# Performance work log

Hardware: AMD Instinct MI355X
Metric: run time of the kernel (lower is better)

Reference implementation:

```python
import jax, jax.numpy as jnp
import numpy as np

N_NODES = 50000
N_EDGES = 800000
IN_FEATS = 128
N_HEADS = 4
OUT_FEATS = 32
NEG_SLOPE = 0.01  # F.leaky_relu default


def setup_inputs() -> dict:
    key = jax.random.key(0)
    k1, k2, k3, k4, k5, k6 = jax.random.split(key, 6)
    feat = jax.random.normal(k1, (N_NODES, IN_FEATS), dtype=jnp.float32)
    src = jax.random.randint(k2, (N_EDGES,), 0, N_NODES, dtype=jnp.int64)
    dst = jax.random.randint(k3, (N_EDGES,), 0, N_NODES, dtype=jnp.int64)
    # xavier-ish scaled params
    W_fc = jax.random.normal(k4, (IN_FEATS, N_HEADS * OUT_FEATS), dtype=jnp.float32) * 0.1
    attn_l = jax.random.normal(k5, (N_HEADS, OUT_FEATS), dtype=jnp.float32) * 0.1
    attn_r = jax.random.normal(k6, (N_HEADS, OUT_FEATS), dtype=jnp.float32) * 0.1
    return {"feat": feat, "src": src, "dst": dst, "W_fc": W_fc,
            "attn_l": attn_l, "attn_r": attn_r}


def reference(feat, src, dst, W_fc, attn_l, attn_r):
    N = feat.shape[0]
    H, D = attn_l.shape
    # fc projection -> [N, H, D]
    h = (feat @ W_fc).reshape(N, H, D)
    # per-node attention logits [N, H]
    el = jnp.einsum('nhd,hd->nh', h, attn_l)
    er = jnp.einsum('nhd,hd->nh', h, attn_r)
    # edge scores: u_add_v then leaky_relu -> [E, H]
    e = jax.nn.leaky_relu(el[src] + er[dst], NEG_SLOPE)
    # faithful to torch.softmax(e, dim=1): softmax over the HEADS axis per edge
    a = jax.nn.softmax(e, axis=1)
    # weighted messages and sum-aggregation over destination nodes
    msg = h[src] * a[:, :, None]                     # [E, H, D]
    rst = jax.ops.segment_sum(msg, dst, num_segments=N)  # [N, H, D]
    # residual: res_fc is Identity since in_feats == H*D
    rst = rst + feat.reshape(N, H, D)
    return jax.nn.elu(rst)
```

## Files before the change

### kernel.cpp

```cpp
#include <hip/hip_runtime.h>

typedef float f32x2 __attribute__((ext_vector_type(2)));
typedef float f32x4 __attribute__((ext_vector_type(4)));
typedef __bf16 bf16x8 __attribute__((ext_vector_type(8)));
typedef unsigned short u16x2 __attribute__((ext_vector_type(2)));
typedef unsigned short u16x4 __attribute__((ext_vector_type(4)));
typedef unsigned short u16x8 __attribute__((ext_vector_type(8)));

#define BSH 5
#define BN 32
#define CAPFIX 1024
#define PNB_MAX 1568
#define SCH 7
#define PCH 4096
#define FC_ROWS 64
#define SMEM_BYTES (4 * PNB_MAX * 4 + PCH * 4 + 256 * 4)

__device__ inline unsigned short f2bf(float x) {
  unsigned int u = __builtin_bit_cast(unsigned int, x);
  unsigned int r = (u + 0x7FFFu + ((u >> 16) & 1u)) >> 16;
  return (unsigned short)r;
}
__device__ inline float bf2f(unsigned short h) {
  unsigned int u = ((unsigned int)h) << 16;
  return __builtin_bit_cast(float, u);
}

__global__ __launch_bounds__(256) void prezero_kernel(const float* __restrict__ W,
                                                      unsigned short* __restrict__ wtp,
                                                      int* __restrict__ bcursor, int n) {
  int b = blockIdx.x;
  if (b < 8) {
    int tid = b * 256 + threadIdx.x;
    int col = tid & 127;
    int kg = tid >> 7;
    float v[8];
#pragma unroll
    for (int j = 0; j < 8; ++j) v[j] = W[(kg * 8 + j) * 128 + col];
    u16x8 pk = {f2bf(v[0]), f2bf(v[1]), f2bf(v[2]), f2bf(v[3]),
                f2bf(v[4]), f2bf(v[5]), f2bf(v[6]), f2bf(v[7])};
    *(u16x8*)&wtp[(size_t)(kg * 128 + col) * 8] = pk;
  } else {
    int i = (b - 8) * 256 + threadIdx.x;
    if (i < n) bcursor[i] = 0;
  }
}

__device__ void partition_body(char* smem, const int* __restrict__ src,
                               const int* __restrict__ dst,
                               int* __restrict__ bcursor, int* __restrict__ tmp,
                               int E, int nbuck, int blk) {
  int* cnt = (int*)smem;
  int* gbase = cnt + PNB_MAX;
  int* lpos = gbase + PNB_MAX;
  int* sbase = lpos + PNB_MAX;
  int* buf = sbase + PNB_MAX;
  int* ts = buf + PCH;
  int t = threadIdx.x;
  int base = blk * PCH;
  int nedge = E - base;
  if (nedge > PCH) nedge = PCH;
  for (int i = t; i < nbuck; i += 256) cnt[i] = 0;
  __syncthreads();
  int rec[16], bb[16];
#pragma unroll
  for (int i = 0; i < 16; ++i) {
    int e = base + t + i * 256;
    bb[i] = -1;
    if (e < E) {
      int d = dst[e];
      int b = d >> BSH;
      bb[i] = b;
      rec[i] = (src[e] & 0xFFFF) | ((d & (BN - 1)) << 16) | (b << 21);
      atomicAdd(&cnt[b], 1);
    }
  }
  __syncthreads();
  for (int i = t; i < nbuck; i += 256) {
    int c = cnt[i];
    gbase[i] = c ? atomicAdd(&bcursor[i], c) : 0;
  }
  {
    int t0 = t * SCH;
    int loc[SCH];
    int s = 0;
#pragma unroll
    for (int j = 0; j < SCH; ++j) {
      int idx = t0 + j;
      loc[j] = s;
      s += (idx < nbuck) ? cnt[idx] : 0;
    }
    ts[t] = s;
    __syncthreads();
    for (int o = 1; o < 256; o <<= 1) {
      int x = (t >= o) ? ts[t - o] : 0;
      __syncthreads();
      ts[t] += x;
      __syncthreads();
    }
    int pre = ts[t] - s;
#pragma unroll
    for (int j = 0; j < SCH; ++j) {
      int idx = t0 + j;
      if (idx < nbuck) {
        int v = pre + loc[j];
        sbase[idx] = v;
        lpos[idx] = v;
      }
    }
  }
  __syncthreads();
#pragma unroll
  for (int i = 0; i < 16; ++i) {
    if (bb[i] >= 0) {
      int p = atomicAdd(&lpos[bb[i]], 1);
      buf[p] = rec[i];
    }
  }
  __syncthreads();
#pragma unroll
  for (int i = 0; i < 16; ++i) {
    int idx = t + i * 256;
    if (idx < nedge) {
      int r = buf[idx];
      int b = (unsigned)r >> 21;
      int off = gbase[b] + (idx - sbase[b]);
      if (off < CAPFIX) tmp[(size_t)b * CAPFIX + off] = r;
    }
  }
}

__device__ void fc_body(char* smem, const float* __restrict__ feat,
                        const unsigned short* __restrict__ wtp,
                        const float* __restrict__ al, const float* __restrict__ ar,
                        unsigned short* __restrict__ hbf,
                        float* __restrict__ el, float* __restrict__ er,
                        int N, int blk) {
  unsigned short* Albs = (unsigned short*)smem;
  int t = threadIdx.x;
  int row0 = blk * FC_ROWS;
#pragma unroll
  for (int i = 0; i < 4; ++i) {
    int ch = i * 256 + t;
    int row = ch >> 4;
    int kg = ch & 15;
    int grow = row0 + row;
    f32x4 x0 = {}, x1 = {};
    if (grow < N) {
      const f32x4* fp = (const f32x4*)(feat + (size_t)grow * 128 + kg * 8);
      x0 = fp[0];
      x1 = fp[1];
    }
    int sc = kg * 64 + (row ^ kg);
    u16x8 pk = {f2bf(x0[0]), f2bf(x0[1]), f2bf(x0[2]), f2bf(x0[3]),
                f2bf(x1[0]), f2bf(x1[1]), f2bf(x1[2]), f2bf(x1[3])};
    *(u16x8*)&Albs[sc * 8] = pk;
  }
  __syncthreads();
  int w = t >> 6;
  int l = t & 63;
  int lr = l & 15;
  int lhi = l >> 4;
  f32x4 acc[8] = {};
  bf16x8 afr[4];
#pragma unroll
  for (int ks = 0; ks < 4; ++ks) {
    int kg = ks * 4 + lhi;
    int row = w * 16 + lr;
    afr[ks] = *(const bf16x8*)&Albs[(kg * 64 + (row ^ kg)) * 8];
  }
#pragma unroll
  for (int nt = 0; nt < 8; ++nt) {
#pragma unroll
    for (int ks = 0; ks < 4; ++ks) {
      int kg = ks * 4 + lhi;
      int col = nt * 16 + lr;
      bf16x8 b = *(const bf16x8*)&wtp[(size_t)(kg * 128 + col) * 8];
      acc[nt] = __builtin_amdgcn_mfma_f32_16x16x32_bf16(afr[ks], b, acc[nt], 0, 0, 0);
    }
  }
#pragma unroll
  for (int nt = 0; nt < 8; ++nt) {
#pragma unroll
    for (int r = 0; r < 4; ++r) {
      int g = row0 + w * 16 + lhi * 4 + r;
      if (g < N) hbf[(size_t)g * 128 + nt * 16 + lr] = f2bf(acc[nt][r]);
    }
  }
  f32x4 pl[4] = {}, pr[4] = {};
#pragma unroll
  for (int nt = 0; nt < 8; ++nt) {
    int hd = nt >> 1;
    float wl = al[nt * 16 + lr];
    float wr = ar[nt * 16 + lr];
#pragma unroll
    for (int r = 0; r < 4; ++r) {
      pl[r][hd] += acc[nt][r] * wl;
      pr[r][hd] += acc[nt][r] * wr;
    }
  }
#pragma unroll
  for (int off = 1; off < 16; off <<= 1) {
#pragma unroll
    for (int r = 0; r < 4; ++r) {
#pragma unroll
      for (int c = 0; c < 4; ++c) {
        pl[r][c] += __shfl_xor(pl[r][c], off);
        pr[r][c] += __shfl_xor(pr[r][c], off);
      }
    }
  }
  if (lr == 0) {
#pragma unroll
    for (int r = 0; r < 4; ++r) {
      int g = row0 + w * 16 + lhi * 4 + r;
      if (g < N) *(f32x4*)(el + (size_t)g * 4) = pl[r];
    }
  } else if (lr == 1) {
#pragma unroll
    for (int r = 0; r < 4; ++r) {
      int g = row0 + w * 16 + lhi * 4 + r;
      if (g < N) *(f32x4*)(er + (size_t)g * 4) = pr[r];
    }
  }
}

__global__ __launch_bounds__(256) void fused_pfc(const int* __restrict__ src,
                                                 const int* __restrict__ dst,
                                                 int* __restrict__ bcursor,
                                                 int* __restrict__ tmp,
                                                 const float* __restrict__ feat,
                                                 const unsigned short* __restrict__ wtp,
                                                 const float* __restrict__ al,
                                                 const float* __restrict__ ar,
                                                 unsigned short* __restrict__ hbf,
                                                 float* __restrict__ el,
                                                 float* __restrict__ er,
                                                 int E, int N, int nbuck, int npart) {
  __shared__ alignas(16) char smem[SMEM_BYTES];
  if ((int)blockIdx.x < npart)
    partition_body(smem, src, dst, bcursor, tmp, E, nbuck, blockIdx.x);
  else
    fc_body(smem, feat, wtp, al, ar, hbf, el, er, N, blockIdx.x - npart);
}

__global__ __launch_bounds__(256) void bucket_gather(const unsigned short* __restrict__ hbf,
                                                     const float* __restrict__ el,
                                                     const float* __restrict__ er,
                                                     const int* __restrict__ bcnt,
                                                     const int* __restrict__ tmp,
                                                     const float* __restrict__ feat,
                                                     float* __restrict__ out, int N) {
  __shared__ unsigned short as_s[CAPFIX];
  __shared__ unsigned short as_a[CAPFIX * 4];
  __shared__ f32x4 er_l[BN];
  __shared__ int cnt[BN], lb[BN], lc2[BN];
  int t = threadIdx.x;
  int bkt = blockIdx.x;
  int nstart = bkt << BSH;
  if (t < BN) {
    int nd = nstart + t;
    f32x4 e4 = {};
    if (nd < N) e4 = *(const f32x4*)(er + (size_t)nd * 4);
    er_l[t] = e4;
    cnt[t] = 0;
    lc2[t] = 0;
  }
  __syncthreads();
  int nrec = min(bcnt[bkt], CAPFIX);
  int myrec[4], mydlo[4];
#pragma unroll
  for (int i = 0; i < 4; ++i) {
    int idx = t + i * 256;
    mydlo[i] = -1;
    if (idx < nrec) {
      int r = tmp[(size_t)bkt * CAPFIX + idx];
      myrec[i] = r;
      int dlo = (r >> 16) & (BN - 1);
      mydlo[i] = dlo;
      atomicAdd(&cnt[dlo], 1);
    }
  }
  __syncthreads();
  if (t < BN) {
    int v = cnt[t];
    int s = v;
#pragma unroll
    for (int o = 1; o < BN; o <<= 1) {
      int x = __shfl_up(s, o, BN);
      if (t >= o) s += x;
    }
    lb[t] = s - v;
  }
  __syncthreads();
#pragma unroll
  for (int i = 0; i < 4; ++i) {
    if (mydlo[i] >= 0) {
      int r = myrec[i];
      int s = r & 0xFFFF;
      int dlo = mydlo[i];
      int p = lb[dlo] + atomicAdd(&lc2[dlo], 1);
      f32x4 l4 = *(const f32x4*)(el + (size_t)s * 4);
      f32x4 r4 = er_l[dlo];
      float e0 = l4[0] + r4[0];
      float e1 = l4[1] + r4[1];
      float e2 = l4[2] + r4[2];
      float e3 = l4[3] + r4[3];
      e0 = e0 > 0.f ? e0 : 0.01f * e0;
      e1 = e1 > 0.f ? e1 : 0.01f * e1;
      e2 = e2 > 0.f ? e2 : 0.01f * e2;
      e3 = e3 > 0.f ? e3 : 0.01f * e3;
      float m = fmaxf(fmaxf(e0, e1), fmaxf(e2, e3));
      float a0 = __expf(e0 - m);
      float a1 = __expf(e1 - m);
      float a2 = __expf(e2 - m);
      float a3 = __expf(e3 - m);
      float inv = 1.0f / (a0 + a1 + a2 + a3);
      u16x4 a = {f2bf(a0 * inv), f2bf(a1 * inv), f2bf(a2 * inv), f2bf(a3 * inv)};
      as_s[p] = (unsigned short)s;
      *(u16x4*)&as_a[p * 4] = a;
    }
  }
  __syncthreads();
  int wv = t >> 6;
  int lane = t & 63;
  int head = lane >> 4;
#pragma unroll
  for (int ni = 0; ni < 8; ++ni) {
    int g = wv * 8 + ni;
    int nd = nstart + g;
    f32x2 acc = {};
    if (nd < N) acc = *(const f32x2*)(feat + (size_t)nd * 128 + lane * 2);
    int st = lb[g], en = st + cnt[g];
    int e = st;
    for (; e + 7 < en; e += 8) {
      f32x2 hx[8];
      float ax[8];
#pragma unroll
      for (int j = 0; j < 8; ++j) {
        int sj = as_s[e + j];
        ax[j] = bf2f(as_a[(e + j) * 4 + head]);
        u16x2 vj = *(const u16x2*)&hbf[(size_t)sj * 128 + lane * 2];
        hx[j] = f32x2{bf2f(vj[0]), bf2f(vj[1])};
      }
#pragma unroll
      for (int j = 0; j < 8; ++j) acc += hx[j] * ax[j];
    }
    for (; e < en; ++e) {
      int s0 = as_s[e];
      float a0 = bf2f(as_a[e * 4 + head]);
      u16x2 v0 = *(const u16x2*)&hbf[(size_t)s0 * 128 + lane * 2];
      acc += f32x2{bf2f(v0[0]), bf2f(v0[1])} * a0;
    }
    if (nd < N) {
      f32x2 o = acc;
      o[0] = o[0] > 0.f ? o[0] : expm1f(o[0]);
      o[1] = o[1] > 0.f ? o[1] : expm1f(o[1]);
      *(f32x2*)(out + (size_t)nd * 128 + lane * 2) = o;
    }
  }
}

extern "C" void kernel_launch(void* const* d_in, const int* in_sizes, int n_in,
                              void* d_out, int out_size, void* d_ws, size_t ws_size,
                              hipStream_t stream) {
  const float* feat = (const float*)d_in[0];
  const int* src = (const int*)d_in[1];
  const int* dst = (const int*)d_in[2];
  const float* W = (const float*)d_in[3];
  const float* al = (const float*)d_in[4];
  const float* ar = (const float*)d_in[5];
  float* out = (float*)d_out;

  int N = in_sizes[0] / 128;
  int E = in_sizes[1];
  int nbuck = (N + BN - 1) >> BSH;

  char* p = (char*)d_ws;
  unsigned short* hbf = (unsigned short*)p; p += (size_t)N * 128 * 2;
  float* el = (float*)p; p += (size_t)N * 4 * 4;
  float* er = (float*)p; p += (size_t)N * 4 * 4;
  unsigned short* wtp = (unsigned short*)p; p += 2048 * 16;
  int* bcursor = (int*)p; p += (size_t)((nbuck + 3) & ~3) * 4;
  int* tmp = (int*)p;

  int npart = (E + PCH - 1) / PCH;
  int nfc = (N + FC_ROWS - 1) / FC_ROWS;

  prezero_kernel<<<8 + (nbuck + 255) / 256, 256, 0, stream>>>(W, wtp, bcursor, nbuck);
  fused_pfc<<<npart + nfc, 256, 0, stream>>>(src, dst, bcursor, tmp, feat, wtp, al, ar,
                                             hbf, el, er, E, N, nbuck, npart);
  bucket_gather<<<nbuck, 256, 0, stream>>>(hbf, el, er, bcursor, tmp, feat, out, N);
}
```

Measured before the change: 70.44 us.

## Gather four edges per wavefront with 16-byte loads and cross-lane reduction

The aggregation loop is restructured so each wavefront processes four edges at once: 16 lanes cover one 128-feature row using 8-element bf16 vector loads, and the four partial sums are combined with xor shuffles. The residual add and ELU are done only by the first lane group using wider stores. This aims to cut per-edge serial iterations and load instruction count, at the cost of shuffle reductions, a masked tail and idle lanes in the epilogue.

```diff
diff --git a/kernel.cpp b/kernel.cpp
--- a/kernel.cpp
+++ b/kernel.cpp
@@ -323,40 +323,65 @@
   }
   __syncthreads();
   int wv = t >> 6;
-  int lane = t & 63;
-  int head = lane >> 4;
+  int l = t & 63;
+  int l4 = l >> 4;
+  int lc = l & 15;
+  int head = lc >> 2;
 #pragma unroll
   for (int ni = 0; ni < 8; ++ni) {
     int g = wv * 8 + ni;
     int nd = nstart + g;
-    f32x2 acc = {};
-    if (nd < N) acc = *(const f32x2*)(feat + (size_t)nd * 128 + lane * 2);
+    f32x4 acc0 = {}, acc1 = {};
     int st = lb[g], en = st + cnt[g];
     int e = st;
-    for (; e + 7 < en; e += 8) {
-      f32x2 hx[8];
-      float ax[8];
-#pragma unroll
-      for (int j = 0; j < 8; ++j) {
-        int sj = as_s[e + j];
-        ax[j] = bf2f(as_a[(e + j) * 4 + head]);
-        u16x2 vj = *(const u16x2*)&hbf[(size_t)sj * 128 + lane * 2];
-        hx[j] = f32x2{bf2f(vj[0]), bf2f(vj[1])};
+    for (; e + 3 < en; e += 4) {
+      int sj = as_s[e + l4];
+      float a = bf2f(as_a[(e + l4) * 4 + head]);
+      u16x8 hv = *(const u16x8*)&hbf[(size_t)sj * 128 + lc * 8];
+      acc0[0] += bf2f(hv[0]) * a;
+      acc0[1] += bf2f(hv[1]) * a;
+      acc0[2] += bf2f(hv[2]) * a;
+      acc0[3] += bf2f(hv[3]) * a;
+      acc1[0] += bf2f(hv[4]) * a;
+      acc1[1] += bf2f(hv[5]) * a;
+      acc1[2] += bf2f(hv[6]) * a;
+      acc1[3] += bf2f(hv[7]) * a;
+    }
+    if (e < en) {
+      int idx = e + l4;
+      bool ok = idx < en;
+      int ii = ok ? idx : st;
+      int sj = as_s[ii];
+      float a = ok ? bf2f(as_a[ii * 4 + head]) : 0.f;
+      u16x8 hv = *(const u16x8*)&hbf[(size_t)sj * 128 + lc * 8];
+      acc0[0] += bf2f(hv[0]) * a;
+      acc0[1] += bf2f(hv[1]) * a;
+      acc0[2] += bf2f(hv[2]) * a;
+      acc0[3] += bf2f(hv[3]) * a;
+      acc1[0] += bf2f(hv[4]) * a;
+      acc1[1] += bf2f(hv[5]) * a;
+      acc1[2] += bf2f(hv[6]) * a;
+      acc1[3] += bf2f(hv[7]) * a;
+    }
+#pragma unroll
+    for (int c = 0; c < 4; ++c) {
+      acc0[c] += __shfl_xor(acc0[c], 16);
+      acc0[c] += __shfl_xor(acc0[c], 32);
+      acc1[c] += __shfl_xor(acc1[c], 16);
+      acc1[c] += __shfl_xor(acc1[c], 32);
+    }
+    if (nd < N && l4 == 0) {
+      const f32x4* fp = (const f32x4*)(feat + (size_t)nd * 128 + lc * 8);
+      f32x4 o0 = acc0 + fp[0];
+      f32x4 o1 = acc1 + fp[1];
+#pragma unroll
+      for (int c = 0; c < 4; ++c) {
+        o0[c] = o0[c] > 0.f ? o0[c] : expm1f(o0[c]);
+        o1[c] = o1[c] > 0.f ? o1[c] : expm1f(o1[c]);
       }
-#pragma unroll
-      for (int j = 0; j < 8; ++j) acc += hx[j] * ax[j];
-    }
-    for (; e < en; ++e) {
-      int s0 = as_s[e];
-      float a0 = bf2f(as_a[e * 4 + head]);
-      u16x2 v0 = *(const u16x2*)&hbf[(size_t)s0 * 128 + lane * 2];
-      acc += f32x2{bf2f(v0[0]), bf2f(v0[1])} * a0;
-    }
-    if (nd < N) {
-      f32x2 o = acc;
-      o[0] = o[0] > 0.f ? o[0] : expm1f(o[0]);
-      o[1] = o[1] > 0.f ? o[1] : expm1f(o[1]);
-      *(f32x2*)(out + (size_t)nd * 128 + lane * 2) = o;
+      f32x4* op = (f32x4*)(out + (size_t)nd * 128 + lc * 8);
+      op[0] = o0;
+      op[1] = o1;
     }
   }
 }
```

Result: slower. 72.98 us (+3.6%).

## Use 512-thread gather blocks with fp32 attention weights and precomputed byte offsets

Applied to the files above, without the earlier changes.

The bucket_gather kernel now runs 512 threads per block (8 waves, 4 destination nodes each) instead of 256 threads with 8 nodes per wave, which gives each block more parallelism and more memory requests in flight. Attention weights are kept in shared memory as fp32 rather than bf16, and source indices are stored as precomputed byte offsets, removing conversion and address arithmetic from the inner loop. The residual feat load moves after the accumulation loop to shorten live ranges. The cost is about twice the shared memory per block, which may reduce the number of resident blocks per CU.

```diff
diff --git a/kernel.cpp b/kernel.cpp
--- a/kernel.cpp
+++ b/kernel.cpp
@@ -4,7 +4,6 @@
 typedef float f32x4 __attribute__((ext_vector_type(4)));
 typedef __bf16 bf16x8 __attribute__((ext_vector_type(8)));
 typedef unsigned short u16x2 __attribute__((ext_vector_type(2)));
-typedef unsigned short u16x4 __attribute__((ext_vector_type(4)));
 typedef unsigned short u16x8 __attribute__((ext_vector_type(8)));
 
 #define BSH 5
@@ -244,15 +243,15 @@
     fc_body(smem, feat, wtp, al, ar, hbf, el, er, N, blockIdx.x - npart);
 }
 
-__global__ __launch_bounds__(256) void bucket_gather(const unsigned short* __restrict__ hbf,
+__global__ __launch_bounds__(512) void bucket_gather(const unsigned short* __restrict__ hbf,
                                                      const float* __restrict__ el,
                                                      const float* __restrict__ er,
                                                      const int* __restrict__ bcnt,
                                                      const int* __restrict__ tmp,
                                                      const float* __restrict__ feat,
                                                      float* __restrict__ out, int N) {
-  __shared__ unsigned short as_s[CAPFIX];
-  __shared__ unsigned short as_a[CAPFIX * 4];
+  __shared__ int as_off[CAPFIX];
+  __shared__ float as_af[CAPFIX * 4];
   __shared__ f32x4 er_l[BN];
   __shared__ int cnt[BN], lb[BN], lc2[BN];
   int t = threadIdx.x;
@@ -268,10 +267,10 @@
   }
   __syncthreads();
   int nrec = min(bcnt[bkt], CAPFIX);
-  int myrec[4], mydlo[4];
-#pragma unroll
-  for (int i = 0; i < 4; ++i) {
-    int idx = t + i * 256;
+  int myrec[2], mydlo[2];
+#pragma unroll
+  for (int i = 0; i < 2; ++i) {
+    int idx = t + i * 512;
     mydlo[i] = -1;
     if (idx < nrec) {
       int r = tmp[(size_t)bkt * CAPFIX + idx];
@@ -294,7 +293,7 @@
   }
   __syncthreads();
 #pragma unroll
-  for (int i = 0; i < 4; ++i) {
+  for (int i = 0; i < 2; ++i) {
     if (mydlo[i] >= 0) {
       int r = myrec[i];
       int s = r & 0xFFFF;
@@ -316,21 +315,20 @@
       float a2 = __expf(e2 - m);
       float a3 = __expf(e3 - m);
       float inv = 1.0f / (a0 + a1 + a2 + a3);
-      u16x4 a = {f2bf(a0 * inv), f2bf(a1 * inv), f2bf(a2 * inv), f2bf(a3 * inv)};
-      as_s[p] = (unsigned short)s;
-      *(u16x4*)&as_a[p * 4] = a;
+      as_off[p] = s << 8;
+      *(f32x4*)&as_af[p * 4] = f32x4{a0 * inv, a1 * inv, a2 * inv, a3 * inv};
     }
   }
   __syncthreads();
   int wv = t >> 6;
-  int lane = t & 63;
-  int head = lane >> 4;
-#pragma unroll
-  for (int ni = 0; ni < 8; ++ni) {
-    int g = wv * 8 + ni;
+  int l = t & 63;
+  int head = l >> 4;
+  const char* hb = (const char*)hbf;
+#pragma unroll
+  for (int ni = 0; ni < 4; ++ni) {
+    int g = wv * 4 + ni;
     int nd = nstart + g;
     f32x2 acc = {};
-    if (nd < N) acc = *(const f32x2*)(feat + (size_t)nd * 128 + lane * 2);
     int st = lb[g], en = st + cnt[g];
     int e = st;
     for (; e + 7 < en; e += 8) {
@@ -338,25 +336,25 @@
       float ax[8];
 #pragma unroll
       for (int j = 0; j < 8; ++j) {
-        int sj = as_s[e + j];
-        ax[j] = bf2f(as_a[(e + j) * 4 + head]);
-        u16x2 vj = *(const u16x2*)&hbf[(size_t)sj * 128 + lane * 2];
+        int off = as_off[e + j];
+        ax[j] = as_af[(e + j) * 4 + head];
+        u16x2 vj = *(const u16x2*)(hb + off + l * 4);
         hx[j] = f32x2{bf2f(vj[0]), bf2f(vj[1])};
       }
 #pragma unroll
       for (int j = 0; j < 8; ++j) acc += hx[j] * ax[j];
     }
     for (; e < en; ++e) {
-      int s0 = as_s[e];
-      float a0 = bf2f(as_a[e * 4 + head]);
-      u16x2 v0 = *(const u16x2*)&hbf[(size_t)s0 * 128 + lane * 2];
+      int off = as_off[e];
+      float a0 = as_af[e * 4 + head];
+      u16x2 v0 = *(const u16x2*)(hb + off + l * 4);
       acc += f32x2{bf2f(v0[0]), bf2f(v0[1])} * a0;
     }
     if (nd < N) {
-      f32x2 o = acc;
+      f32x2 o = acc + *(const f32x2*)(feat + (size_t)nd * 128 + l * 2);
       o[0] = o[0] > 0.f ? o[0] : expm1f(o[0]);
       o[1] = o[1] > 0.f ? o[1] : expm1f(o[1]);
-      *(f32x2*)(out + (size_t)nd * 128 + lane * 2) = o;
+      *(f32x2*)(out + (size_t)nd * 128 + l * 2) = o;
     }
   }
 }
@@ -390,5 +388,5 @@
   prezero_kernel<<<8 + (nbuck + 255) / 256, 256, 0, stream>>>(W, wtp, bcursor, nbuck);
   fused_pfc<<<npart + nfc, 256, 0, stream>>>(src, dst, bcursor, tmp, feat, wtp, al, ar,
                                              hbf, el, er, E, N, nbuck, npart);
-  bucket_gather<<<nbuck, 256, 0, stream>>>(hbf, el, er, bcursor, tmp, feat, out, N);
-}
+  bucket_gather<<<nbuck, 512, 0, stream>>>(hbf, el, er, bcursor, tmp, feat, out, N);
+}
```

Measured after the change: 71.28 us. No clear change (+1.2%).
